# Kernel tuning notes

Hardware: AMD Instinct MI355X
Metric: run time of the kernel (lower is better)

Reference implementation:

```python
import jax, jax.numpy as jnp
import numpy as np

B, H, S, D = 2, 16, 2048, 64

def setup_inputs() -> dict:
    key = jax.random.key(0)
    kq, kk, kv = jax.random.split(key, 3)
    q = jax.random.normal(kq, (B, H, S, D), dtype=jnp.float32)
    k = jax.random.normal(kk, (B, H, S, D), dtype=jnp.float32)
    v = jax.random.normal(kv, (B, H, S, D), dtype=jnp.float32)
    # additive causal mask: 0 on/below diagonal, -1e9 above
    causal = jnp.tril(jnp.ones((S, S), dtype=bool))
    mask = jnp.where(causal, 0.0, -1e9).astype(jnp.float32)[None, None]
    return {"q": q, "k": k, "v": v, "mask": mask}

def reference(q, k, v, mask):
    # scores: [B,H,Sq,Sk]
    scale = 1.0 / jnp.sqrt(jnp.asarray(k.shape[-1], dtype=q.dtype))
    scores = jnp.einsum("bhqd,bhkd->bhqk", q, k) * scale
    scores = scores + mask
    attn = jax.nn.softmax(scores, axis=-1)
    return jnp.einsum("bhqk,bhkd->bhqd", attn, v)
```

## Files before the change

### kernel.cpp

```cpp
#include <hip/hip_runtime.h>
#include <hip/hip_bf16.h>


#define S_LEN 2048
#define D_DIM 64
#define BQ 64
#define BKV 64
#define NQT (S_LEN / BQ)
#define NBH 32

typedef __bf16 bf16x8 __attribute__((ext_vector_type(8)));
typedef __bf16 bf16x4 __attribute__((ext_vector_type(4)));
typedef float f32x4 __attribute__((ext_vector_type(4)));

#define QSCALE 0.1803368801111243f
#define NEG_INF (-1e30f)
#define THRLOG2 11.5f

__device__ inline void glds16(const void* g, void* l) {
    __builtin_amdgcn_global_load_lds(
        (const __attribute__((address_space(1))) unsigned int*)g,
        (__attribute__((address_space(3))) unsigned int*)l, 16, 0, 0);
}

__device__ inline float m3(float a, float b, float c) {
    return fmaxf(fmaxf(a, b), c);
}

__global__ __launch_bounds__(256)
void conv_fused_kernel(const float* __restrict__ k, const float* __restrict__ v,
                       __bf16* __restrict__ kb, __bf16* __restrict__ vt)
{
    __shared__ __bf16 T[64][72];
    const int bh = blockIdx.y, st = blockIdx.x;
    const int tid = threadIdx.x;
    const size_t base = (size_t)bh * S_LEN * D_DIM + (size_t)st * 64 * D_DIM;
    const float* kh = k + base;
    const float* vh = v + base;
    __bf16* kbh = kb + base;

#pragma unroll
    for (int it = 0; it < 2; ++it) {
        size_t i = ((size_t)tid + it * 256) * 8;
        float4 a = *(const float4*)(kh + i);
        float4 b = *(const float4*)(kh + i + 4);
        bf16x8 o;
        o[0] = (__bf16)a.x; o[1] = (__bf16)a.y; o[2] = (__bf16)a.z; o[3] = (__bf16)a.w;
        o[4] = (__bf16)b.x; o[5] = (__bf16)b.y; o[6] = (__bf16)b.z; o[7] = (__bf16)b.w;
        *(bf16x8*)(kbh + i) = o;
    }

#pragma unroll
    for (int it = 0; it < 4; ++it) {
        int idx = tid + it * 256;
        int s = idx >> 4, c4 = idx & 15;
        float4 f = *(const float4*)(vh + s * D_DIM + c4 * 4);
        T[c4 * 4 + 0][s] = (__bf16)f.x;
        T[c4 * 4 + 1][s] = (__bf16)f.y;
        T[c4 * 4 + 2][s] = (__bf16)f.z;
        T[c4 * 4 + 3][s] = (__bf16)f.w;
    }
    __syncthreads();
    __bf16* vth = vt + (size_t)bh * D_DIM * S_LEN + st * 64;
#pragma unroll
    for (int it = 0; it < 2; ++it) {
        int idx = tid + it * 256;
        int d = idx >> 3, c8 = idx & 7;
        int kk = c8 >> 2, g = c8 & 3;
        bf16x4 v0 = *(const bf16x4*)&T[d][kk * 32 + 4 * g];
        bf16x4 v1 = *(const bf16x4*)&T[d][kk * 32 + 16 + 4 * g];
        bf16x8 o;
        o[0] = v0[0]; o[1] = v0[1]; o[2] = v0[2]; o[3] = v0[3];
        o[4] = v1[0]; o[5] = v1[1]; o[6] = v1[2]; o[7] = v1[3];
        *(bf16x8*)(vth + (size_t)d * S_LEN + c8 * 8) = o;
    }
}


#define STAGE(kt, buf)                                                          \
    {                                                                           \
        _Pragma("unroll")                                                       \
        for (int u = 0; u < 2; ++u) {                                           \
            glds16(kh + (size_t)((kt) * BKV + row_u[u]) * D_DIM + scol_u[u],    \
                   (__bf16*)&KL[buf][0][0] + (u * 4 + w) * 512);                \
            glds16(vh + (size_t)row_u[u] * S_LEN + (kt) * BKV + scol_u[u],      \
                   (__bf16*)&VL[buf][0][0] + (u * 4 + w) * 512);                \
        }                                                                       \
    }

__global__ __launch_bounds__(256)
void attn_fwd_split(const float* __restrict__ q, const __bf16* __restrict__ kb,
                    const __bf16* __restrict__ vt, float* __restrict__ opart,
                    float* __restrict__ ml)
{
    __shared__ __bf16 KL[2][64][64];
    __shared__ __bf16 VL[2][64][64];

    const int tid  = threadIdx.x;
    const int w    = tid >> 6;
    const int lane = tid & 63;
    const int l15  = lane & 15;
    const int lg   = lane >> 4;

    const int ph = blockIdx.x;
    const int p  = ph >> 1;
    const int h  = ph & 1;
    const int bh = blockIdx.y;

    const float*  qh = q  + (size_t)bh * S_LEN * D_DIM;
    const __bf16* kh = kb + (size_t)bh * S_LEN * D_DIM;
    const __bf16* vh = vt + (size_t)bh * D_DIM * S_LEN;

    int row_u[2], scol_u[2];
#pragma unroll
    for (int u = 0; u < 2; ++u) {
        int e = (u * 4 + w) * 512 + lane * 8;
        int r = e >> 6, c0 = e & 63;
        row_u[u]  = r;
        scol_u[u] = c0 ^ ((r & 7) << 3);
    }

    for (int half = 0; half < 2; ++half) {
        const int qtile = (half == 0) ? (NQT - 1 - p) : p;
        const int qbase = qtile * BQ;
        const int cnt   = (qtile >= h) ? (((qtile - h) >> 1) + 1) : 0;

        bf16x8 qf[2];
        {
            const int qrow = qbase + w * 16 + l15;
            const float* qp = qh + (size_t)qrow * D_DIM + 8 * lg;
#pragma unroll
            for (int kk = 0; kk < 2; ++kk) {
                float4 a = *(const float4*)(qp + kk * 32);
                float4 b = *(const float4*)(qp + kk * 32 + 4);
                bf16x8 f;
                f[0] = (__bf16)(a.x * QSCALE); f[1] = (__bf16)(a.y * QSCALE);
                f[2] = (__bf16)(a.z * QSCALE); f[3] = (__bf16)(a.w * QSCALE);
                f[4] = (__bf16)(b.x * QSCALE); f[5] = (__bf16)(b.y * QSCALE);
                f[6] = (__bf16)(b.z * QSCALE); f[7] = (__bf16)(b.w * QSCALE);
                qf[kk] = f;
            }
        }

        f32x4 acc[4] = {};
        float m_run = NEG_INF;
        float l_part = 0.0f;

        if (half == 1) __syncthreads();
        if (cnt > 0) STAGE(h, 0);

        for (int i = 0; i < cnt; ++i) {
            const int kt  = h + 2 * i;
            const int cur = i & 1;
            asm volatile("s_waitcnt vmcnt(0)" ::: "memory");
            __builtin_amdgcn_s_barrier();
            if (i + 1 < cnt) STAGE(kt + 2, cur ^ 1);

            f32x4 s[4];
            __builtin_amdgcn_s_setprio(1);
#pragma unroll
            for (int jt = 0; jt < 4; ++jt) {
                const int j  = jt * 16 + l15;
                const int sw = (j & 7) << 3;
                f32x4 c = {};
#pragma unroll
                for (int kk = 0; kk < 2; ++kk) {
                    bf16x8 kf = *(const bf16x8*)&KL[cur][j][(kk * 32 + 8 * lg) ^ sw];
                    c = __builtin_amdgcn_mfma_f32_16x16x32_bf16(kf, qf[kk], c, 0, 0, 0);
                }
                s[jt] = c;
            }
            __builtin_amdgcn_s_setprio(0);

            if (kt == qtile) {
                const int qin = w * 16 + l15;
#pragma unroll
                for (int jt = 0; jt < 4; ++jt)
#pragma unroll
                    for (int r = 0; r < 4; ++r)
                        if (jt * 16 + 4 * lg + r > qin) s[jt][r] = NEG_INF;
            }

            float t0 = m3(s[0][0], s[0][1], s[0][2]);
            float t1 = m3(s[0][3], s[1][0], s[1][1]);
            float t2 = m3(s[1][2], s[1][3], s[2][0]);
            float t3 = m3(s[2][1], s[2][2], s[2][3]);
            float t4 = m3(s[3][0], s[3][1], s[3][2]);
            float mxl = m3(m3(t0, t1, t2), m3(t3, t4, s[3][3]), NEG_INF);

            if (__any(mxl > m_run + THRLOG2)) {
                float mx = fmaxf(mxl, __shfl_xor(mxl, 16));
                mx = fmaxf(mx, __shfl_xor(mx, 32));
                const float mt   = fmaxf(m_run, mx);
                const float corr = __builtin_amdgcn_exp2f(m_run - mt);
                l_part *= corr;
                m_run   = mt;
                float corr_a[4];
#pragma unroll
                for (int r = 0; r < 4; ++r) corr_a[r] = __shfl(corr, 4 * lg + r);
#pragma unroll
                for (int dt = 0; dt < 4; ++dt)
#pragma unroll
                    for (int r = 0; r < 4; ++r) acc[dt][r] *= corr_a[r];
            }

            float ps = 0.0f;
            float pe[4][4];
#pragma unroll
            for (int jt = 0; jt < 4; ++jt)
#pragma unroll
                for (int r = 0; r < 4; ++r) {
                    float e = __builtin_amdgcn_exp2f(s[jt][r] - m_run);
                    pe[jt][r] = e;
                    ps += e;
                }
            l_part += ps;

            bf16x8 pa[2];
#pragma unroll
            for (int kk = 0; kk < 2; ++kk)
#pragma unroll
                for (int i2 = 0; i2 < 4; ++i2) {
                    pa[kk][i2]     = (__bf16)pe[2 * kk][i2];
                    pa[kk][4 + i2] = (__bf16)pe[2 * kk + 1][i2];
                }

            __builtin_amdgcn_s_setprio(1);
#pragma unroll
            for (int dt = 0; dt < 4; ++dt) {
                const int d  = dt * 16 + l15;
                const int sw = (d & 7) << 3;
#pragma unroll
                for (int kk = 0; kk < 2; ++kk) {
                    bf16x8 vb = *(const bf16x8*)&VL[cur][d][(kk * 32 + 8 * lg) ^ sw];
                    acc[dt] = __builtin_amdgcn_mfma_f32_16x16x32_bf16(pa[kk], vb, acc[dt], 0, 0, 0);
                }
            }
            __builtin_amdgcn_s_setprio(0);
        }

        float l_tot = l_part + __shfl_xor(l_part, 16);
        l_tot += __shfl_xor(l_tot, 32);

        float* op = opart + ((((size_t)bh * NQT + qtile) * 2 + h) << 12);
#pragma unroll
        for (int dt = 0; dt < 4; ++dt)
#pragma unroll
            for (int r = 0; r < 4; ++r)
                op[(w * 16 + 4 * lg + r) * 64 + dt * 16 + l15] = acc[dt][r];

        if (lg == 0) {
            float* mlp = ml + ((((size_t)bh * NQT + qtile) * 2 + h) << 7);
            mlp[w * 16 + l15]      = m_run;
            mlp[64 + w * 16 + l15] = l_tot;
        }
    }
}


__global__ __launch_bounds__(256)
void combine_kernel(const float* __restrict__ opart, const float* __restrict__ ml,
                    float* __restrict__ out)
{
    const int qt  = blockIdx.x;
    const int bh  = blockIdx.y;
    const int tid = threadIdx.x;
    const int row = tid >> 2;
    const int c16 = (tid & 3) * 16;

    const float* ml0 = ml + ((((size_t)bh * NQT + qt) * 2) << 7);
    const float* ml1 = ml0 + 128;
    const float m0 = ml0[row], l0 = ml0[64 + row];
    const float m1 = ml1[row], l1 = ml1[64 + row];
    const float M  = fmaxf(m0, m1);
    const float w0 = __builtin_amdgcn_exp2f(m0 - M);
    const float w1 = __builtin_amdgcn_exp2f(m1 - M);
    const float li = __builtin_amdgcn_rcpf(w0 * l0 + w1 * l1);

    const float* o0 = opart + ((((size_t)bh * NQT + qt) * 2) << 12) + row * 64 + c16;
    const float* o1 = o0 + 4096;
    float* oh = out + ((size_t)bh * S_LEN + qt * 64 + row) * D_DIM + c16;
#pragma unroll
    for (int c = 0; c < 4; ++c) {
        float4 a = ((const float4*)o0)[c];
        float4 b = ((const float4*)o1)[c];
        float4 o;
        o.x = (a.x * w0 + b.x * w1) * li;
        o.y = (a.y * w0 + b.y * w1) * li;
        o.z = (a.z * w0 + b.z * w1) * li;
        o.w = (a.w * w0 + b.w * w1) * li;
        ((float4*)oh)[c] = o;
    }
}


__global__ __launch_bounds__(256)
void attn_fwd_glds(const float* __restrict__ q, const __bf16* __restrict__ kb,
                   const __bf16* __restrict__ vt, float* __restrict__ out)
{
    __shared__ __bf16 KL[3][64][64];
    __shared__ __bf16 VL[3][64][64];

    const int tid  = threadIdx.x;
    const int w    = tid >> 6;
    const int lane = tid & 63;
    const int l15  = lane & 15;
    const int lg   = lane >> 4;

    const int p  = blockIdx.x;
    const int bh = blockIdx.y;

    const float*  qh = q  + (size_t)bh * S_LEN * D_DIM;
    const __bf16* kh = kb + (size_t)bh * S_LEN * D_DIM;
    const __bf16* vh = vt + (size_t)bh * D_DIM * S_LEN;
    float*        oh = out + (size_t)bh * S_LEN * D_DIM;

    int row_u[2], scol_u[2];
#pragma unroll
    for (int u = 0; u < 2; ++u) {
        int e = (u * 4 + w) * 512 + lane * 8;
        int r = e >> 6, c0 = e & 63;
        row_u[u]  = r;
        scol_u[u] = c0 ^ ((r & 7) << 3);
    }

    for (int half = 0; half < 2; ++half) {
        const int qtile = (half == 0) ? (NQT - 1 - p) : p;
        const int qbase = qtile * BQ;
        const int nt    = qtile + 1;

        bf16x8 qf[2];
        {
            const int qrow = qbase + w * 16 + l15;
            const float* qp = qh + (size_t)qrow * D_DIM + 8 * lg;
#pragma unroll
            for (int kk = 0; kk < 2; ++kk) {
                float4 a = *(const float4*)(qp + kk * 32);
                float4 b = *(const float4*)(qp + kk * 32 + 4);
                bf16x8 f;
                f[0] = (__bf16)(a.x * QSCALE); f[1] = (__bf16)(a.y * QSCALE);
                f[2] = (__bf16)(a.z * QSCALE); f[3] = (__bf16)(a.w * QSCALE);
                f[4] = (__bf16)(b.x * QSCALE); f[5] = (__bf16)(b.y * QSCALE);
                f[6] = (__bf16)(b.z * QSCALE); f[7] = (__bf16)(b.w * QSCALE);
                qf[kk] = f;
            }
        }

        f32x4 acc[4] = {};
        float m_run = NEG_INF;
        float l_part = 0.0f;

        if (half == 1) __syncthreads();
        STAGE(0, 0);
        if (nt > 1) STAGE(1, 1);

        for (int kt = 0; kt < nt; ++kt) {
            const int cur = kt % 3;
            if (kt + 1 < nt) { asm volatile("s_waitcnt vmcnt(4)" ::: "memory"); }
            else             { asm volatile("s_waitcnt vmcnt(0)" ::: "memory"); }
            __builtin_amdgcn_s_barrier();
            if (kt + 2 < nt) STAGE(kt + 2, (kt + 2) % 3);

            f32x4 s[4];
            __builtin_amdgcn_s_setprio(1);
#pragma unroll
            for (int jt = 0; jt < 4; ++jt) {
                const int j  = jt * 16 + l15;
                const int sw = (j & 7) << 3;
                f32x4 c = {};
#pragma unroll
                for (int kk = 0; kk < 2; ++kk) {
                    bf16x8 kf = *(const bf16x8*)&KL[cur][j][(kk * 32 + 8 * lg) ^ sw];
                    c = __builtin_amdgcn_mfma_f32_16x16x32_bf16(kf, qf[kk], c, 0, 0, 0);
                }
                s[jt] = c;
            }
            __builtin_amdgcn_s_setprio(0);

            if (kt == qtile) {
                const int qin = w * 16 + l15;
#pragma unroll
                for (int jt = 0; jt < 4; ++jt)
#pragma unroll
                    for (int r = 0; r < 4; ++r)
                        if (jt * 16 + 4 * lg + r > qin) s[jt][r] = NEG_INF;
            }

            float t0 = m3(s[0][0], s[0][1], s[0][2]);
            float t1 = m3(s[0][3], s[1][0], s[1][1]);
            float t2 = m3(s[1][2], s[1][3], s[2][0]);
            float t3 = m3(s[2][1], s[2][2], s[2][3]);
            float t4 = m3(s[3][0], s[3][1], s[3][2]);
            float mxl = m3(m3(t0, t1, t2), m3(t3, t4, s[3][3]), NEG_INF);

            if (__any(mxl > m_run + THRLOG2)) {
                float mx = fmaxf(mxl, __shfl_xor(mxl, 16));
                mx = fmaxf(mx, __shfl_xor(mx, 32));
                const float mt   = fmaxf(m_run, mx);
                const float corr = __builtin_amdgcn_exp2f(m_run - mt);
                l_part *= corr;
                m_run   = mt;
                float corr_a[4];
#pragma unroll
                for (int r = 0; r < 4; ++r) corr_a[r] = __shfl(corr, 4 * lg + r);
#pragma unroll
                for (int dt = 0; dt < 4; ++dt)
#pragma unroll
                    for (int r = 0; r < 4; ++r) acc[dt][r] *= corr_a[r];
            }

            float ps = 0.0f;
            float pe[4][4];
#pragma unroll
            for (int jt = 0; jt < 4; ++jt)
#pragma unroll
                for (int r = 0; r < 4; ++r) {
                    float e = __builtin_amdgcn_exp2f(s[jt][r] - m_run);
                    pe[jt][r] = e;
                    ps += e;
                }
            l_part += ps;

            bf16x8 pa[2];
#pragma unroll
            for (int kk = 0; kk < 2; ++kk)
#pragma unroll
                for (int i = 0; i < 4; ++i) {
                    pa[kk][i]     = (__bf16)pe[2 * kk][i];
                    pa[kk][4 + i] = (__bf16)pe[2 * kk + 1][i];
                }

            __builtin_amdgcn_s_setprio(1);
#pragma unroll
            for (int dt = 0; dt < 4; ++dt) {
                const int d  = dt * 16 + l15;
                const int sw = (d & 7) << 3;
#pragma unroll
                for (int kk = 0; kk < 2; ++kk) {
                    bf16x8 vb = *(const bf16x8*)&VL[cur][d][(kk * 32 + 8 * lg) ^ sw];
                    acc[dt] = __builtin_amdgcn_mfma_f32_16x16x32_bf16(pa[kk], vb, acc[dt], 0, 0, 0);
                }
            }
            __builtin_amdgcn_s_setprio(0);
        }

        float l_tot = l_part + __shfl_xor(l_part, 16);
        l_tot += __shfl_xor(l_tot, 32);
        float li_a[4];
#pragma unroll
        for (int r = 0; r < 4; ++r)
            li_a[r] = __builtin_amdgcn_rcpf(__shfl(l_tot, 4 * lg + r));
#pragma unroll
        for (int dt = 0; dt < 4; ++dt)
#pragma unroll
            for (int r = 0; r < 4; ++r)
                oh[(size_t)(qbase + w * 16 + 4 * lg + r) * D_DIM + dt * 16 + l15] =
                    acc[dt][r] * li_a[r];
    }
}
#undef STAGE


#define PAD 72
__global__ __launch_bounds__(256)
void attn_fwd_fallback(const float* __restrict__ q, const float* __restrict__ k,
                       const float* __restrict__ v, float* __restrict__ out)
{
    __shared__ __bf16 Klds[64][PAD];
    __shared__ __bf16 Vt[D_DIM][PAD];
    __shared__ __bf16 Plds[4][16][PAD];

    const int tid  = threadIdx.x;
    const int w    = tid >> 6;
    const int lane = tid & 63;
    const int l15  = lane & 15;
    const int lg   = lane >> 4;

    const int qtile = blockIdx.x;
    const int bh    = blockIdx.y;
    const int qbase = qtile * 64;

    const size_t head_off = (size_t)bh * S_LEN * D_DIM;
    const float* qh = q + head_off;
    const float* kh = k + head_off;
    const float* vh = v + head_off;
    float*       oh = out + head_off;

    bf16x8 qf[2];
    {
        const int qrow = qbase + w * 16 + l15;
        const float* qp = qh + (size_t)qrow * D_DIM + 8 * lg;
#pragma unroll
        for (int c = 0; c < 2; ++c) {
            float4 a = *(const float4*)(qp + c * 32);
            float4 b = *(const float4*)(qp + c * 32 + 4);
            bf16x8 f;
            f[0] = (__bf16)(a.x * 0.125f); f[1] = (__bf16)(a.y * 0.125f);
            f[2] = (__bf16)(a.z * 0.125f); f[3] = (__bf16)(a.w * 0.125f);
            f[4] = (__bf16)(b.x * 0.125f); f[5] = (__bf16)(b.y * 0.125f);
            f[6] = (__bf16)(b.z * 0.125f); f[7] = (__bf16)(b.w * 0.125f);
            qf[c] = f;
        }
    }

    f32x4 acc[4] = {};
    float m_run[4], l_run[4];
#pragma unroll
    for (int r = 0; r < 4; ++r) { m_run[r] = -1e30f; l_run[r] = 0.0f; }

    const int nkv = qtile + 1;
    for (int kt = 0; kt < nkv; ++kt) {
        const int kv0 = kt * 64;
        __syncthreads();
#pragma unroll
        for (int it = 0; it < 4; ++it) {
            int idx = tid + it * 256;
            int row = idx >> 4;
            int c4  = idx & 15;
            float4 kf = *(const float4*)(kh + (size_t)(kv0 + row) * D_DIM + c4 * 4);
            __bf16* kd = &Klds[row][c4 * 4];
            kd[0] = (__bf16)kf.x; kd[1] = (__bf16)kf.y;
            kd[2] = (__bf16)kf.z; kd[3] = (__bf16)kf.w;
            float4 vf = *(const float4*)(vh + (size_t)(kv0 + row) * D_DIM + c4 * 4);
            Vt[c4 * 4 + 0][row] = (__bf16)vf.x;
            Vt[c4 * 4 + 1][row] = (__bf16)vf.y;
            Vt[c4 * 4 + 2][row] = (__bf16)vf.z;
            Vt[c4 * 4 + 3][row] = (__bf16)vf.w;
        }
        __syncthreads();

        f32x4 sfrag[4];
#pragma unroll
        for (int kc = 0; kc < 4; ++kc) {
            bf16x8 kf0 = *(const bf16x8*)&Klds[kc * 16 + l15][8 * lg];
            bf16x8 kf1 = *(const bf16x8*)&Klds[kc * 16 + l15][32 + 8 * lg];
            f32x4 c = {};
            c = __builtin_amdgcn_mfma_f32_16x16x32_bf16(qf[0], kf0, c, 0, 0, 0);
            c = __builtin_amdgcn_mfma_f32_16x16x32_bf16(qf[1], kf1, c, 0, 0, 0);
            sfrag[kc] = c;
        }

        if (kt == qtile) {
#pragma unroll
            for (int kc = 0; kc < 4; ++kc) {
                const int j = kv0 + kc * 16 + l15;
#pragma unroll
                for (int r = 0; r < 4; ++r) {
                    const int qrow = qbase + w * 16 + lg * 4 + r;
                    if (j > qrow) sfrag[kc][r] = -1e30f;
                }
            }
        }

        float mt[4], corr[4], ps[4];
#pragma unroll
        for (int r = 0; r < 4; ++r) {
            float mx = fmaxf(fmaxf(sfrag[0][r], sfrag[1][r]),
                             fmaxf(sfrag[2][r], sfrag[3][r]));
            mx = fmaxf(mx, __shfl_xor(mx, 1));
            mx = fmaxf(mx, __shfl_xor(mx, 2));
            mx = fmaxf(mx, __shfl_xor(mx, 4));
            mx = fmaxf(mx, __shfl_xor(mx, 8));
            mt[r]   = fmaxf(m_run[r], mx);
            corr[r] = __expf(m_run[r] - mt[r]);
            ps[r]   = 0.0f;
        }
#pragma unroll
        for (int kc = 0; kc < 4; ++kc) {
#pragma unroll
            for (int r = 0; r < 4; ++r) {
                float pp = __expf(sfrag[kc][r] - mt[r]);
                ps[r] += pp;
                Plds[w][lg * 4 + r][kc * 16 + l15] = (__bf16)pp;
            }
        }
#pragma unroll
        for (int r = 0; r < 4; ++r) {
            ps[r] += __shfl_xor(ps[r], 1);
            ps[r] += __shfl_xor(ps[r], 2);
            ps[r] += __shfl_xor(ps[r], 4);
            ps[r] += __shfl_xor(ps[r], 8);
            l_run[r] = l_run[r] * corr[r] + ps[r];
            m_run[r] = mt[r];
        }
#pragma unroll
        for (int dt = 0; dt < 4; ++dt)
#pragma unroll
            for (int r = 0; r < 4; ++r)
                acc[dt][r] *= corr[r];

#pragma unroll
        for (int kk = 0; kk < 2; ++kk) {
            bf16x8 pf = *(const bf16x8*)&Plds[w][l15][kk * 32 + 8 * lg];
#pragma unroll
            for (int dt = 0; dt < 4; ++dt) {
                bf16x8 vf = *(const bf16x8*)&Vt[dt * 16 + l15][kk * 32 + 8 * lg];
                acc[dt] = __builtin_amdgcn_mfma_f32_16x16x32_bf16(pf, vf, acc[dt], 0, 0, 0);
            }
        }
    }

#pragma unroll
    for (int dt = 0; dt < 4; ++dt) {
#pragma unroll
        for (int r = 0; r < 4; ++r) {
            const int qrow = qbase + w * 16 + lg * 4 + r;
            oh[(size_t)qrow * D_DIM + dt * 16 + l15] = acc[dt][r] / l_run[r];
        }
    }
}

extern "C" void kernel_launch(void* const* d_in, const int* in_sizes, int n_in,
                              void* d_out, int out_size, void* d_ws, size_t ws_size,
                              hipStream_t stream) {
    const float* q = (const float*)d_in[0];
    const float* k = (const float*)d_in[1];
    const float* v = (const float*)d_in[2];
    float* out = (float*)d_out;

    const size_t kv_elems   = (size_t)NBH * S_LEN * D_DIM;
    const size_t conv_bytes = kv_elems * 2 * sizeof(__bf16);
    const size_t op_bytes   = (size_t)NBH * NQT * 2 * 4096 * 4;
    const size_t ml_bytes   = (size_t)NBH * NQT * 2 * 128 * 4;

    if (ws_size >= conv_bytes + op_bytes + ml_bytes) {
        __bf16* kb = (__bf16*)d_ws;
        __bf16* vt = kb + kv_elems;
        float* opart = (float*)((char*)d_ws + conv_bytes);
        float* ml    = (float*)((char*)d_ws + conv_bytes + op_bytes);
        conv_fused_kernel<<<dim3(S_LEN / 64, NBH), dim3(256), 0, stream>>>(k, v, kb, vt);
        attn_fwd_split<<<dim3(32, NBH), dim3(256), 0, stream>>>(q, kb, vt, opart, ml);
        combine_kernel<<<dim3(NQT, NBH), dim3(256), 0, stream>>>(opart, ml, out);
    } else if (ws_size >= conv_bytes) {
        __bf16* kb = (__bf16*)d_ws;
        __bf16* vt = kb + kv_elems;
        conv_fused_kernel<<<dim3(S_LEN / 64, NBH), dim3(256), 0, stream>>>(k, v, kb, vt);
        attn_fwd_glds<<<dim3(NQT / 2, NBH), dim3(256), 0, stream>>>(q, kb, vt, out);
    } else {
        attn_fwd_fallback<<<dim3(S_LEN / 64, NBH), dim3(256), 0, stream>>>(q, k, v, out);
    }
}
```

Baseline: 60.33 us.

## Split attention into one q-tile per block, triple-buffer KV, store partials as bf16

Each block of the split kernel now handles a single query tile and KV parity instead of a paired long and short tile, doubling the grid to 64x32 blocks. The K/V LDS staging moves from double to triple buffering with a partial vmcnt wait, so two tiles are in flight. Partial outputs are stored as bf16 rather than fp32, which halves the partial write and combine read traffic. The cost is less even per-block work across the causal triangle, more LDS per block, and some extra rounding of the partial outputs.

```diff
diff --git a/kernel.cpp b/kernel.cpp
--- a/kernel.cpp
+++ b/kernel.cpp
@@ -90,11 +90,11 @@
 
 __global__ __launch_bounds__(256)
 void attn_fwd_split(const float* __restrict__ q, const __bf16* __restrict__ kb,
-                    const __bf16* __restrict__ vt, float* __restrict__ opart,
+                    const __bf16* __restrict__ vt, __bf16* __restrict__ opart,
                     float* __restrict__ ml)
 {
-    __shared__ __bf16 KL[2][64][64];
-    __shared__ __bf16 VL[2][64][64];
+    __shared__ __bf16 KL[3][64][64];
+    __shared__ __bf16 VL[3][64][64];
 
     const int tid  = threadIdx.x;
     const int w    = tid >> 6;
@@ -102,10 +102,12 @@
     const int l15  = lane & 15;
     const int lg   = lane >> 4;
 
-    const int ph = blockIdx.x;
-    const int p  = ph >> 1;
-    const int h  = ph & 1;
-    const int bh = blockIdx.y;
+    const int u0    = blockIdx.x;
+    const int qtile = NQT - 1 - (u0 >> 1);
+    const int h     = u0 & 1;
+    const int bh    = blockIdx.y;
+    const int qbase = qtile * BQ;
+    const int cnt   = (qtile >= h) ? (((qtile - h) >> 1) + 1) : 0;
 
     const float*  qh = q  + (size_t)bh * S_LEN * D_DIM;
     const __bf16* kh = kb + (size_t)bh * S_LEN * D_DIM;
@@ -120,146 +122,141 @@
         scol_u[u] = c0 ^ ((r & 7) << 3);
     }
 
-    for (int half = 0; half < 2; ++half) {
-        const int qtile = (half == 0) ? (NQT - 1 - p) : p;
-        const int qbase = qtile * BQ;
-        const int cnt   = (qtile >= h) ? (((qtile - h) >> 1) + 1) : 0;
-
-        bf16x8 qf[2];
-        {
-            const int qrow = qbase + w * 16 + l15;
-            const float* qp = qh + (size_t)qrow * D_DIM + 8 * lg;
+    bf16x8 qf[2];
+    {
+        const int qrow = qbase + w * 16 + l15;
+        const float* qp = qh + (size_t)qrow * D_DIM + 8 * lg;
+#pragma unroll
+        for (int kk = 0; kk < 2; ++kk) {
+            float4 a = *(const float4*)(qp + kk * 32);
+            float4 b = *(const float4*)(qp + kk * 32 + 4);
+            bf16x8 f;
+            f[0] = (__bf16)(a.x * QSCALE); f[1] = (__bf16)(a.y * QSCALE);
+            f[2] = (__bf16)(a.z * QSCALE); f[3] = (__bf16)(a.w * QSCALE);
+            f[4] = (__bf16)(b.x * QSCALE); f[5] = (__bf16)(b.y * QSCALE);
+            f[6] = (__bf16)(b.z * QSCALE); f[7] = (__bf16)(b.w * QSCALE);
+            qf[kk] = f;
+        }
+    }
+
+    f32x4 acc[4] = {};
+    float m_run = NEG_INF;
+    float l_part = 0.0f;
+
+    if (cnt > 0) STAGE(h, 0);
+    if (cnt > 1) STAGE(h + 2, 1);
+
+    for (int i = 0; i < cnt; ++i) {
+        const int kt  = h + 2 * i;
+        const int cur = i % 3;
+        if (i + 1 < cnt) { asm volatile("s_waitcnt vmcnt(4)" ::: "memory"); }
+        else             { asm volatile("s_waitcnt vmcnt(0)" ::: "memory"); }
+        __builtin_amdgcn_s_barrier();
+        if (i + 2 < cnt) STAGE(h + 2 * (i + 2), (i + 2) % 3);
+
+        f32x4 s[4];
+        __builtin_amdgcn_s_setprio(1);
+#pragma unroll
+        for (int jt = 0; jt < 4; ++jt) {
+            const int j  = jt * 16 + l15;
+            const int sw = (j & 7) << 3;
+            f32x4 c = {};
 #pragma unroll
             for (int kk = 0; kk < 2; ++kk) {
-                float4 a = *(const float4*)(qp + kk * 32);
-                float4 b = *(const float4*)(qp + kk * 32 + 4);
-                bf16x8 f;
-                f[0] = (__bf16)(a.x * QSCALE); f[1] = (__bf16)(a.y * QSCALE);
-                f[2] = (__bf16)(a.z * QSCALE); f[3] = (__bf16)(a.w * QSCALE);
-                f[4] = (__bf16)(b.x * QSCALE); f[5] = (__bf16)(b.y * QSCALE);
-                f[6] = (__bf16)(b.z * QSCALE); f[7] = (__bf16)(b.w * QSCALE);
-                qf[kk] = f;
-            }
-        }
-
-        f32x4 acc[4] = {};
-        float m_run = NEG_INF;
-        float l_part = 0.0f;
-
-        if (half == 1) __syncthreads();
-        if (cnt > 0) STAGE(h, 0);
-
-        for (int i = 0; i < cnt; ++i) {
-            const int kt  = h + 2 * i;
-            const int cur = i & 1;
-            asm volatile("s_waitcnt vmcnt(0)" ::: "memory");
-            __builtin_amdgcn_s_barrier();
-            if (i + 1 < cnt) STAGE(kt + 2, cur ^ 1);
-
-            f32x4 s[4];
-            __builtin_amdgcn_s_setprio(1);
-#pragma unroll
-            for (int jt = 0; jt < 4; ++jt) {
-                const int j  = jt * 16 + l15;
-                const int sw = (j & 7) << 3;
-                f32x4 c = {};
-#pragma unroll
-                for (int kk = 0; kk < 2; ++kk) {
-                    bf16x8 kf = *(const bf16x8*)&KL[cur][j][(kk * 32 + 8 * lg) ^ sw];
-                    c = __builtin_amdgcn_mfma_f32_16x16x32_bf16(kf, qf[kk], c, 0, 0, 0);
-                }
-                s[jt] = c;
-            }
-            __builtin_amdgcn_s_setprio(0);
-
-            if (kt == qtile) {
-                const int qin = w * 16 + l15;
-#pragma unroll
-                for (int jt = 0; jt < 4; ++jt)
-#pragma unroll
-                    for (int r = 0; r < 4; ++r)
-                        if (jt * 16 + 4 * lg + r > qin) s[jt][r] = NEG_INF;
-            }
-
-            float t0 = m3(s[0][0], s[0][1], s[0][2]);
-            float t1 = m3(s[0][3], s[1][0], s[1][1]);
-            float t2 = m3(s[1][2], s[1][3], s[2][0]);
-            float t3 = m3(s[2][1], s[2][2], s[2][3]);
-            float t4 = m3(s[3][0], s[3][1], s[3][2]);
-            float mxl = m3(m3(t0, t1, t2), m3(t3, t4, s[3][3]), NEG_INF);
-
-            if (__any(mxl > m_run + THRLOG2)) {
-                float mx = fmaxf(mxl, __shfl_xor(mxl, 16));
-                mx = fmaxf(mx, __shfl_xor(mx, 32));
-                const float mt   = fmaxf(m_run, mx);
-                const float corr = __builtin_amdgcn_exp2f(m_run - mt);
-                l_part *= corr;
-                m_run   = mt;
-                float corr_a[4];
-#pragma unroll
-                for (int r = 0; r < 4; ++r) corr_a[r] = __shfl(corr, 4 * lg + r);
-#pragma unroll
-                for (int dt = 0; dt < 4; ++dt)
-#pragma unroll
-                    for (int r = 0; r < 4; ++r) acc[dt][r] *= corr_a[r];
-            }
-
-            float ps = 0.0f;
-            float pe[4][4];
+                bf16x8 kf = *(const bf16x8*)&KL[cur][j][(kk * 32 + 8 * lg) ^ sw];
+                c = __builtin_amdgcn_mfma_f32_16x16x32_bf16(kf, qf[kk], c, 0, 0, 0);
+            }
+            s[jt] = c;
+        }
+        __builtin_amdgcn_s_setprio(0);
+
+        if (kt == qtile) {
+            const int qin = w * 16 + l15;
 #pragma unroll
             for (int jt = 0; jt < 4; ++jt)
 #pragma unroll
-                for (int r = 0; r < 4; ++r) {
-                    float e = __builtin_amdgcn_exp2f(s[jt][r] - m_run);
-                    pe[jt][r] = e;
-                    ps += e;
-                }
-            l_part += ps;
-
-            bf16x8 pa[2];
-#pragma unroll
-            for (int kk = 0; kk < 2; ++kk)
-#pragma unroll
-                for (int i2 = 0; i2 < 4; ++i2) {
-                    pa[kk][i2]     = (__bf16)pe[2 * kk][i2];
-                    pa[kk][4 + i2] = (__bf16)pe[2 * kk + 1][i2];
-                }
-
-            __builtin_amdgcn_s_setprio(1);
-#pragma unroll
-            for (int dt = 0; dt < 4; ++dt) {
-                const int d  = dt * 16 + l15;
-                const int sw = (d & 7) << 3;
-#pragma unroll
-                for (int kk = 0; kk < 2; ++kk) {
-                    bf16x8 vb = *(const bf16x8*)&VL[cur][d][(kk * 32 + 8 * lg) ^ sw];
-                    acc[dt] = __builtin_amdgcn_mfma_f32_16x16x32_bf16(pa[kk], vb, acc[dt], 0, 0, 0);
-                }
-            }
-            __builtin_amdgcn_s_setprio(0);
-        }
-
-        float l_tot = l_part + __shfl_xor(l_part, 16);
-        l_tot += __shfl_xor(l_tot, 32);
-
-        float* op = opart + ((((size_t)bh * NQT + qtile) * 2 + h) << 12);
-#pragma unroll
-        for (int dt = 0; dt < 4; ++dt)
-#pragma unroll
-            for (int r = 0; r < 4; ++r)
-                op[(w * 16 + 4 * lg + r) * 64 + dt * 16 + l15] = acc[dt][r];
-
-        if (lg == 0) {
-            float* mlp = ml + ((((size_t)bh * NQT + qtile) * 2 + h) << 7);
-            mlp[w * 16 + l15]      = m_run;
-            mlp[64 + w * 16 + l15] = l_tot;
-        }
+                for (int r = 0; r < 4; ++r)
+                    if (jt * 16 + 4 * lg + r > qin) s[jt][r] = NEG_INF;
+        }
+
+        float t0 = m3(s[0][0], s[0][1], s[0][2]);
+        float t1 = m3(s[0][3], s[1][0], s[1][1]);
+        float t2 = m3(s[1][2], s[1][3], s[2][0]);
+        float t3 = m3(s[2][1], s[2][2], s[2][3]);
+        float t4 = m3(s[3][0], s[3][1], s[3][2]);
+        float mxl = m3(m3(t0, t1, t2), m3(t3, t4, s[3][3]), NEG_INF);
+
+        if (__any(mxl > m_run + THRLOG2)) {
+            float mx = fmaxf(mxl, __shfl_xor(mxl, 16));
+            mx = fmaxf(mx, __shfl_xor(mx, 32));
+            const float mt   = fmaxf(m_run, mx);
+            const float corr = __builtin_amdgcn_exp2f(m_run - mt);
+            l_part *= corr;
+            m_run   = mt;
+            float corr_a[4];
+#pragma unroll
+            for (int r = 0; r < 4; ++r) corr_a[r] = __shfl(corr, 4 * lg + r);
+#pragma unroll
+            for (int dt = 0; dt < 4; ++dt)
+#pragma unroll
+                for (int r = 0; r < 4; ++r) acc[dt][r] *= corr_a[r];
+        }
+
+        float ps = 0.0f;
+        float pe[4][4];
+#pragma unroll
+        for (int jt = 0; jt < 4; ++jt)
+#pragma unroll
+            for (int r = 0; r < 4; ++r) {
+                float e = __builtin_amdgcn_exp2f(s[jt][r] - m_run);
+                pe[jt][r] = e;
+                ps += e;
+            }
+        l_part += ps;
+
+        bf16x8 pa[2];
+#pragma unroll
+        for (int kk = 0; kk < 2; ++kk)
+#pragma unroll
+            for (int i2 = 0; i2 < 4; ++i2) {
+                pa[kk][i2]     = (__bf16)pe[2 * kk][i2];
+                pa[kk][4 + i2] = (__bf16)pe[2 * kk + 1][i2];
+            }
+
+        __builtin_amdgcn_s_setprio(1);
+#pragma unroll
+        for (int dt = 0; dt < 4; ++dt) {
+            const int d  = dt * 16 + l15;
+            const int sw = (d & 7) << 3;
+#pragma unroll
+            for (int kk = 0; kk < 2; ++kk) {
+                bf16x8 vb = *(const bf16x8*)&VL[cur][d][(kk * 32 + 8 * lg) ^ sw];
+                acc[dt] = __builtin_amdgcn_mfma_f32_16x16x32_bf16(pa[kk], vb, acc[dt], 0, 0, 0);
+            }
+        }
+        __builtin_amdgcn_s_setprio(0);
+    }
+
+    float l_tot = l_part + __shfl_xor(l_part, 16);
+    l_tot += __shfl_xor(l_tot, 32);
+
+    __bf16* op = opart + ((((size_t)bh * NQT + qtile) * 2 + h) << 12);
+#pragma unroll
+    for (int dt = 0; dt < 4; ++dt)
+#pragma unroll
+        for (int r = 0; r < 4; ++r)
+            op[(w * 16 + 4 * lg + r) * 64 + dt * 16 + l15] = (__bf16)acc[dt][r];
+
+    if (lg == 0) {
+        float* mlp = ml + ((((size_t)bh * NQT + qtile) * 2 + h) << 7);
+        mlp[w * 16 + l15]      = m_run;
+        mlp[64 + w * 16 + l15] = l_tot;
     }
 }
 
 
 __global__ __launch_bounds__(256)
-void combine_kernel(const float* __restrict__ opart, const float* __restrict__ ml,
+void combine_kernel(const __bf16* __restrict__ opart, const float* __restrict__ ml,
                     float* __restrict__ out)
 {
     const int qt  = blockIdx.x;
@@ -277,20 +274,23 @@
     const float w1 = __builtin_amdgcn_exp2f(m1 - M);
     const float li = __builtin_amdgcn_rcpf(w0 * l0 + w1 * l1);
 
-    const float* o0 = opart + ((((size_t)bh * NQT + qt) * 2) << 12) + row * 64 + c16;
-    const float* o1 = o0 + 4096;
+    const __bf16* o0 = opart + ((((size_t)bh * NQT + qt) * 2) << 12) + row * 64 + c16;
+    const __bf16* o1 = o0 + 4096;
+    bf16x8 a0 = *(const bf16x8*)o0;
+    bf16x8 a1 = *(const bf16x8*)(o0 + 8);
+    bf16x8 b0 = *(const bf16x8*)o1;
+    bf16x8 b1 = *(const bf16x8*)(o1 + 8);
+
     float* oh = out + ((size_t)bh * S_LEN + qt * 64 + row) * D_DIM + c16;
-#pragma unroll
-    for (int c = 0; c < 4; ++c) {
-        float4 a = ((const float4*)o0)[c];
-        float4 b = ((const float4*)o1)[c];
-        float4 o;
-        o.x = (a.x * w0 + b.x * w1) * li;
-        o.y = (a.y * w0 + b.y * w1) * li;
-        o.z = (a.z * w0 + b.z * w1) * li;
-        o.w = (a.w * w0 + b.w * w1) * li;
-        ((float4*)oh)[c] = o;
-    }
+    float res[16];
+#pragma unroll
+    for (int j = 0; j < 8; ++j) {
+        res[j]     = ((float)a0[j] * w0 + (float)b0[j] * w1) * li;
+        res[8 + j] = ((float)a1[j] * w0 + (float)b1[j] * w1) * li;
+    }
+#pragma unroll
+    for (int c = 0; c < 4; ++c)
+        ((float4*)oh)[c] = make_float4(res[c*4], res[c*4+1], res[c*4+2], res[c*4+3]);
 }
 
 
@@ -620,16 +620,16 @@
 
     const size_t kv_elems   = (size_t)NBH * S_LEN * D_DIM;
     const size_t conv_bytes = kv_elems * 2 * sizeof(__bf16);
-    const size_t op_bytes   = (size_t)NBH * NQT * 2 * 4096 * 4;
+    const size_t op_bytes   = (size_t)NBH * NQT * 2 * 4096 * 2;
     const size_t ml_bytes   = (size_t)NBH * NQT * 2 * 128 * 4;
 
     if (ws_size >= conv_bytes + op_bytes + ml_bytes) {
         __bf16* kb = (__bf16*)d_ws;
         __bf16* vt = kb + kv_elems;
-        float* opart = (float*)((char*)d_ws + conv_bytes);
-        float* ml    = (float*)((char*)d_ws + conv_bytes + op_bytes);
+        __bf16* opart = (__bf16*)((char*)d_ws + conv_bytes);
+        float*  ml    = (float*)((char*)d_ws + conv_bytes + op_bytes);
         conv_fused_kernel<<<dim3(S_LEN / 64, NBH), dim3(256), 0, stream>>>(k, v, kb, vt);
-        attn_fwd_split<<<dim3(32, NBH), dim3(256), 0, stream>>>(q, kb, vt, opart, ml);
+        attn_fwd_split<<<dim3(64, NBH), dim3(256), 0, stream>>>(q, kb, vt, opart, ml);
         combine_kernel<<<dim3(NQT, NBH), dim3(256), 0, stream>>>(opart, ml, out);
     } else if (ws_size >= conv_bytes) {
         __bf16* kb = (__bf16*)d_ws;
```

Measured after the change: 70.62 us. 1.17x slower.

## Use 128-row Q tiles per block in split attention with bf16 partial outputs

Applied to the files above, without the earlier changes.

The split attention kernel now processes 128 query rows per block, with each wave handling two 16-row chunks. Each K/V tile loaded into LDS is therefore reused across twice as many queries, and the paired-tile load balancing is replaced by launching the longest tiles first. Partial outputs are stored as bf16 instead of fp32 to halve the workspace traffic into the combine kernel, and launch bounds now request 4 blocks per SM. The trade-offs are higher register pressure and some extra rounding error in the partial outputs.

```diff
diff --git a/kernel.cpp b/kernel.cpp
--- a/kernel.cpp
+++ b/kernel.cpp
@@ -4,17 +4,17 @@
 
 #define S_LEN 2048
 #define D_DIM 64
-#define BQ 64
 #define BKV 64
-#define NQT (S_LEN / BQ)
 #define NBH 32
+#define NT128 16
 
 typedef __bf16 bf16x8 __attribute__((ext_vector_type(8)));
 typedef __bf16 bf16x4 __attribute__((ext_vector_type(4)));
 typedef float f32x4 __attribute__((ext_vector_type(4)));
 
 #define QSCALE 0.1803368801111243f
-#define NEG_INF (-1e30f)
+#define NEG_MASK (-1e30f)
+#define M_INIT  (-1e29f)
 #define THRLOG2 11.5f
 
 __device__ inline void glds16(const void* g, void* l) {
@@ -88,9 +88,10 @@
         }                                                                       \
     }
 
-__global__ __launch_bounds__(256)
+
+__global__ __launch_bounds__(256, 4)
 void attn_fwd_split(const float* __restrict__ q, const __bf16* __restrict__ kb,
-                    const __bf16* __restrict__ vt, float* __restrict__ opart,
+                    const __bf16* __restrict__ vt, __bf16* __restrict__ opart,
                     float* __restrict__ ml)
 {
     __shared__ __bf16 KL[2][64][64];
@@ -102,10 +103,12 @@
     const int l15  = lane & 15;
     const int lg   = lane >> 4;
 
-    const int ph = blockIdx.x;
-    const int p  = ph >> 1;
-    const int h  = ph & 1;
+    const int u0 = blockIdx.x;
+    const int T  = NT128 - 1 - (u0 >> 1);
+    const int h  = u0 & 1;
     const int bh = blockIdx.y;
+    const int qbase = T * 128;
+    const int cnt   = T + 1;
 
     const float*  qh = q  + (size_t)bh * S_LEN * D_DIM;
     const __bf16* kh = kb + (size_t)bh * S_LEN * D_DIM;
@@ -120,10 +123,244 @@
         scol_u[u] = c0 ^ ((r & 7) << 3);
     }
 
+    bf16x8 qf[2][2];
+#pragma unroll
+    for (int qc = 0; qc < 2; ++qc) {
+        const int qrow = qbase + w * 32 + qc * 16 + l15;
+        const float* qp = qh + (size_t)qrow * D_DIM + 8 * lg;
+#pragma unroll
+        for (int kk = 0; kk < 2; ++kk) {
+            float4 a = *(const float4*)(qp + kk * 32);
+            float4 b = *(const float4*)(qp + kk * 32 + 4);
+            bf16x8 f;
+            f[0] = (__bf16)(a.x * QSCALE); f[1] = (__bf16)(a.y * QSCALE);
+            f[2] = (__bf16)(a.z * QSCALE); f[3] = (__bf16)(a.w * QSCALE);
+            f[4] = (__bf16)(b.x * QSCALE); f[5] = (__bf16)(b.y * QSCALE);
+            f[6] = (__bf16)(b.z * QSCALE); f[7] = (__bf16)(b.w * QSCALE);
+            qf[qc][kk] = f;
+        }
+    }
+
+    f32x4 acc[4][2] = {};
+    float m_run[2]  = {M_INIT, M_INIT};
+    float l_part[2] = {0.0f, 0.0f};
+
+    STAGE(h, 0);
+
+    for (int i = 0; i < cnt; ++i) {
+        const int kt  = h + 2 * i;
+        const int cur = i & 1;
+        asm volatile("s_waitcnt vmcnt(0)" ::: "memory");
+        __builtin_amdgcn_s_barrier();
+        if (i + 1 < cnt) STAGE(kt + 2, cur ^ 1);
+
+        bf16x8 kf[4][2];
+#pragma unroll
+        for (int jt = 0; jt < 4; ++jt) {
+            const int j  = jt * 16 + l15;
+            const int sw = (j & 7) << 3;
+            kf[jt][0] = *(const bf16x8*)&KL[cur][j][(8 * lg) ^ sw];
+            kf[jt][1] = *(const bf16x8*)&KL[cur][j][(32 + 8 * lg) ^ sw];
+        }
+
+        f32x4 s0[4], s1[4];
+        __builtin_amdgcn_s_setprio(1);
+#pragma unroll
+        for (int jt = 0; jt < 4; ++jt) {
+            f32x4 c = {};
+            c = __builtin_amdgcn_mfma_f32_16x16x32_bf16(kf[jt][0], qf[0][0], c, 0, 0, 0);
+            c = __builtin_amdgcn_mfma_f32_16x16x32_bf16(kf[jt][1], qf[0][1], c, 0, 0, 0);
+            s0[jt] = c;
+            f32x4 d = {};
+            d = __builtin_amdgcn_mfma_f32_16x16x32_bf16(kf[jt][0], qf[1][0], d, 0, 0, 0);
+            d = __builtin_amdgcn_mfma_f32_16x16x32_bf16(kf[jt][1], qf[1][1], d, 0, 0, 0);
+            s1[jt] = d;
+        }
+        __builtin_amdgcn_s_setprio(0);
+
+        if (i == cnt - 1) {
+            const int q0 = w * 32 + l15;
+#pragma unroll
+            for (int jt = 0; jt < 4; ++jt)
+#pragma unroll
+                for (int r = 0; r < 4; ++r) {
+                    const int jl = h * 64 + jt * 16 + 4 * lg + r;
+                    if (jl > q0)      s0[jt][r] = NEG_MASK;
+                    if (jl > q0 + 16) s1[jt][r] = NEG_MASK;
+                }
+        }
+
+        float mxl0, mxl1;
+        {
+            float t0 = m3(s0[0][0], s0[0][1], s0[0][2]);
+            float t1 = m3(s0[0][3], s0[1][0], s0[1][1]);
+            float t2 = m3(s0[1][2], s0[1][3], s0[2][0]);
+            float t3 = m3(s0[2][1], s0[2][2], s0[2][3]);
+            float t4 = m3(s0[3][0], s0[3][1], s0[3][2]);
+            mxl0 = m3(m3(t0, t1, t2), m3(t3, t4, s0[3][3]), NEG_MASK);
+            float u1 = m3(s1[0][0], s1[0][1], s1[0][2]);
+            float u2 = m3(s1[0][3], s1[1][0], s1[1][1]);
+            float u3 = m3(s1[1][2], s1[1][3], s1[2][0]);
+            float u4 = m3(s1[2][1], s1[2][2], s1[2][3]);
+            float u5 = m3(s1[3][0], s1[3][1], s1[3][2]);
+            mxl1 = m3(m3(u1, u2, u3), m3(u4, u5, s1[3][3]), NEG_MASK);
+        }
+
+        if (__any((mxl0 > m_run[0] + THRLOG2) || (mxl1 > m_run[1] + THRLOG2))) {
+            float mx0 = fmaxf(mxl0, __shfl_xor(mxl0, 16));
+            mx0 = fmaxf(mx0, __shfl_xor(mx0, 32));
+            float mx1 = fmaxf(mxl1, __shfl_xor(mxl1, 16));
+            mx1 = fmaxf(mx1, __shfl_xor(mx1, 32));
+            const float mt0 = fmaxf(m_run[0], mx0);
+            const float mt1 = fmaxf(m_run[1], mx1);
+            const float c0 = __builtin_amdgcn_exp2f(m_run[0] - mt0);
+            const float c1 = __builtin_amdgcn_exp2f(m_run[1] - mt1);
+            l_part[0] *= c0; m_run[0] = mt0;
+            l_part[1] *= c1; m_run[1] = mt1;
+            float ca0[4], ca1[4];
+#pragma unroll
+            for (int r = 0; r < 4; ++r) {
+                ca0[r] = __shfl(c0, 4 * lg + r);
+                ca1[r] = __shfl(c1, 4 * lg + r);
+            }
+#pragma unroll
+            for (int dt = 0; dt < 4; ++dt)
+#pragma unroll
+                for (int r = 0; r < 4; ++r) {
+                    acc[dt][0][r] *= ca0[r];
+                    acc[dt][1][r] *= ca1[r];
+                }
+        }
+
+        float ps0 = 0.0f, ps1 = 0.0f;
+        bf16x8 pa0[2], pa1[2];
+#pragma unroll
+        for (int kk = 0; kk < 2; ++kk)
+#pragma unroll
+            for (int i2 = 0; i2 < 4; ++i2) {
+                float ea = __builtin_amdgcn_exp2f(s0[2 * kk][i2] - m_run[0]);
+                float eb = __builtin_amdgcn_exp2f(s0[2 * kk + 1][i2] - m_run[0]);
+                ps0 += ea + eb;
+                pa0[kk][i2]     = (__bf16)ea;
+                pa0[kk][4 + i2] = (__bf16)eb;
+                float fa = __builtin_amdgcn_exp2f(s1[2 * kk][i2] - m_run[1]);
+                float fb = __builtin_amdgcn_exp2f(s1[2 * kk + 1][i2] - m_run[1]);
+                ps1 += fa + fb;
+                pa1[kk][i2]     = (__bf16)fa;
+                pa1[kk][4 + i2] = (__bf16)fb;
+            }
+        l_part[0] += ps0;
+        l_part[1] += ps1;
+
+        __builtin_amdgcn_s_setprio(1);
+#pragma unroll
+        for (int dt = 0; dt < 4; ++dt) {
+            const int d  = dt * 16 + l15;
+            const int sw = (d & 7) << 3;
+#pragma unroll
+            for (int kk = 0; kk < 2; ++kk) {
+                bf16x8 vb = *(const bf16x8*)&VL[cur][d][(kk * 32 + 8 * lg) ^ sw];
+                acc[dt][0] = __builtin_amdgcn_mfma_f32_16x16x32_bf16(pa0[kk], vb, acc[dt][0], 0, 0, 0);
+                acc[dt][1] = __builtin_amdgcn_mfma_f32_16x16x32_bf16(pa1[kk], vb, acc[dt][1], 0, 0, 0);
+            }
+        }
+        __builtin_amdgcn_s_setprio(0);
+    }
+
+    __bf16* op  = opart + ((((size_t)bh * NT128 + T) * 2 + h) << 13);
+    float*  mlp = ml    + ((((size_t)bh * NT128 + T) * 2 + h) << 8);
+#pragma unroll
+    for (int qc = 0; qc < 2; ++qc) {
+        float lt = l_part[qc] + __shfl_xor(l_part[qc], 16);
+        lt += __shfl_xor(lt, 32);
+#pragma unroll
+        for (int dt = 0; dt < 4; ++dt)
+#pragma unroll
+            for (int r = 0; r < 4; ++r)
+                op[(w * 32 + qc * 16 + 4 * lg + r) * 64 + dt * 16 + l15] =
+                    (__bf16)acc[dt][qc][r];
+        if (lg == 0) {
+            mlp[w * 32 + qc * 16 + l15]       = m_run[qc];
+            mlp[128 + w * 32 + qc * 16 + l15] = lt;
+        }
+    }
+}
+
+
+__global__ __launch_bounds__(256)
+void combine_kernel(const __bf16* __restrict__ opart, const float* __restrict__ ml,
+                    float* __restrict__ out)
+{
+    const int T   = blockIdx.x;
+    const int bh  = blockIdx.y;
+    const int tid = threadIdx.x;
+    const int row = tid >> 1;
+    const int c0  = (tid & 1) * 32;
+
+    const float* mlp = ml + (((size_t)bh * NT128 + T) * 2 << 8);
+    const float m0 = mlp[row],       l0 = mlp[128 + row];
+    const float m1 = mlp[256 + row], l1 = mlp[384 + row];
+    const float M  = fmaxf(m0, m1);
+    const float w0 = __builtin_amdgcn_exp2f(m0 - M);
+    const float w1 = __builtin_amdgcn_exp2f(m1 - M);
+    const float li = __builtin_amdgcn_rcpf(w0 * l0 + w1 * l1);
+
+    const __bf16* o0 = opart + (((size_t)bh * NT128 + T) * 2 << 13) + row * 64 + c0;
+    const __bf16* o1 = o0 + 8192;
+    float* oh = out + ((size_t)bh * S_LEN + T * 128 + row) * D_DIM + c0;
+#pragma unroll
+    for (int cc = 0; cc < 4; ++cc) {
+        bf16x8 a = *(const bf16x8*)(o0 + cc * 8);
+        bf16x8 b = *(const bf16x8*)(o1 + cc * 8);
+        float4 r0, r1;
+        r0.x = ((float)a[0] * w0 + (float)b[0] * w1) * li;
+        r0.y = ((float)a[1] * w0 + (float)b[1] * w1) * li;
+        r0.z = ((float)a[2] * w0 + (float)b[2] * w1) * li;
+        r0.w = ((float)a[3] * w0 + (float)b[3] * w1) * li;
+        r1.x = ((float)a[4] * w0 + (float)b[4] * w1) * li;
+        r1.y = ((float)a[5] * w0 + (float)b[5] * w1) * li;
+        r1.z = ((float)a[6] * w0 + (float)b[6] * w1) * li;
+        r1.w = ((float)a[7] * w0 + (float)b[7] * w1) * li;
+        ((float4*)(oh + cc * 8))[0] = r0;
+        ((float4*)(oh + cc * 8))[1] = r1;
+    }
+}
+
+
+__global__ __launch_bounds__(256)
+void attn_fwd_glds(const float* __restrict__ q, const __bf16* __restrict__ kb,
+                   const __bf16* __restrict__ vt, float* __restrict__ out)
+{
+    __shared__ __bf16 KL[3][64][64];
+    __shared__ __bf16 VL[3][64][64];
+
+    const int tid  = threadIdx.x;
+    const int w    = tid >> 6;
+    const int lane = tid & 63;
+    const int l15  = lane & 15;
+    const int lg   = lane >> 4;
+
+    const int p  = blockIdx.x;
+    const int bh = blockIdx.y;
+
+    const float*  qh = q  + (size_t)bh * S_LEN * D_DIM;
+    const __bf16* kh = kb + (size_t)bh * S_LEN * D_DIM;
+    const __bf16* vh = vt + (size_t)bh * D_DIM * S_LEN;
+    float*        oh = out + (size_t)bh * S_LEN * D_DIM;
+
+    int row_u[2], scol_u[2];
+#pragma unroll
+    for (int u = 0; u < 2; ++u) {
+        int e = (u * 4 + w) * 512 + lane * 8;
+        int r = e >> 6, c0 = e & 63;
+        row_u[u]  = r;
+        scol_u[u] = c0 ^ ((r & 7) << 3);
+    }
+
     for (int half = 0; half < 2; ++half) {
-        const int qtile = (half == 0) ? (NQT - 1 - p) : p;
-        const int qbase = qtile * BQ;
-        const int cnt   = (qtile >= h) ? (((qtile - h) >> 1) + 1) : 0;
+        const int qtile = (half == 0) ? (31 - p) : p;
+        const int qbase = qtile * 64;
+        const int nt    = qtile + 1;
 
         bf16x8 qf[2];
         {
@@ -143,211 +380,7 @@
         }
 
         f32x4 acc[4] = {};
-        float m_run = NEG_INF;
-        float l_part = 0.0f;
-
-        if (half == 1) __syncthreads();
-        if (cnt > 0) STAGE(h, 0);
-
-        for (int i = 0; i < cnt; ++i) {
-            const int kt  = h + 2 * i;
-            const int cur = i & 1;
-            asm volatile("s_waitcnt vmcnt(0)" ::: "memory");
-            __builtin_amdgcn_s_barrier();
-            if (i + 1 < cnt) STAGE(kt + 2, cur ^ 1);
-
-            f32x4 s[4];
-            __builtin_amdgcn_s_setprio(1);
-#pragma unroll
-            for (int jt = 0; jt < 4; ++jt) {
-                const int j  = jt * 16 + l15;
-                const int sw = (j & 7) << 3;
-                f32x4 c = {};
-#pragma unroll
-                for (int kk = 0; kk < 2; ++kk) {
-                    bf16x8 kf = *(const bf16x8*)&KL[cur][j][(kk * 32 + 8 * lg) ^ sw];
-                    c = __builtin_amdgcn_mfma_f32_16x16x32_bf16(kf, qf[kk], c, 0, 0, 0);
-                }
-                s[jt] = c;
-            }
-            __builtin_amdgcn_s_setprio(0);
-
-            if (kt == qtile) {
-                const int qin = w * 16 + l15;
-#pragma unroll
-                for (int jt = 0; jt < 4; ++jt)
-#pragma unroll
-                    for (int r = 0; r < 4; ++r)
-                        if (jt * 16 + 4 * lg + r > qin) s[jt][r] = NEG_INF;
-            }
-
-            float t0 = m3(s[0][0], s[0][1], s[0][2]);
-            float t1 = m3(s[0][3], s[1][0], s[1][1]);
-            float t2 = m3(s[1][2], s[1][3], s[2][0]);
-            float t3 = m3(s[2][1], s[2][2], s[2][3]);
-            float t4 = m3(s[3][0], s[3][1], s[3][2]);
-            float mxl = m3(m3(t0, t1, t2), m3(t3, t4, s[3][3]), NEG_INF);
-
-            if (__any(mxl > m_run + THRLOG2)) {
-                float mx = fmaxf(mxl, __shfl_xor(mxl, 16));
-                mx = fmaxf(mx, __shfl_xor(mx, 32));
-                const float mt   = fmaxf(m_run, mx);
-                const float corr = __builtin_amdgcn_exp2f(m_run - mt);
-                l_part *= corr;
-                m_run   = mt;
-                float corr_a[4];
-#pragma unroll
-                for (int r = 0; r < 4; ++r) corr_a[r] = __shfl(corr, 4 * lg + r);
-#pragma unroll
-                for (int dt = 0; dt < 4; ++dt)
-#pragma unroll
-                    for (int r = 0; r < 4; ++r) acc[dt][r] *= corr_a[r];
-            }
-
-            float ps = 0.0f;
-            float pe[4][4];
-#pragma unroll
-            for (int jt = 0; jt < 4; ++jt)
-#pragma unroll
-                for (int r = 0; r < 4; ++r) {
-                    float e = __builtin_amdgcn_exp2f(s[jt][r] - m_run);
-                    pe[jt][r] = e;
-                    ps += e;
-                }
-            l_part += ps;
-
-            bf16x8 pa[2];
-#pragma unroll
-            for (int kk = 0; kk < 2; ++kk)
-#pragma unroll
-                for (int i2 = 0; i2 < 4; ++i2) {
-                    pa[kk][i2]     = (__bf16)pe[2 * kk][i2];
-                    pa[kk][4 + i2] = (__bf16)pe[2 * kk + 1][i2];
-                }
-
-            __builtin_amdgcn_s_setprio(1);
-#pragma unroll
-            for (int dt = 0; dt < 4; ++dt) {
-                const int d  = dt * 16 + l15;
-                const int sw = (d & 7) << 3;
-#pragma unroll
-                for (int kk = 0; kk < 2; ++kk) {
-                    bf16x8 vb = *(const bf16x8*)&VL[cur][d][(kk * 32 + 8 * lg) ^ sw];
-                    acc[dt] = __builtin_amdgcn_mfma_f32_16x16x32_bf16(pa[kk], vb, acc[dt], 0, 0, 0);
-                }
-            }
-            __builtin_amdgcn_s_setprio(0);
-        }
-
-        float l_tot = l_part + __shfl_xor(l_part, 16);
-        l_tot += __shfl_xor(l_tot, 32);
-
-        float* op = opart + ((((size_t)bh * NQT + qtile) * 2 + h) << 12);
-#pragma unroll
-        for (int dt = 0; dt < 4; ++dt)
-#pragma unroll
-            for (int r = 0; r < 4; ++r)
-                op[(w * 16 + 4 * lg + r) * 64 + dt * 16 + l15] = acc[dt][r];
-
-        if (lg == 0) {
-            float* mlp = ml + ((((size_t)bh * NQT + qtile) * 2 + h) << 7);
-            mlp[w * 16 + l15]      = m_run;
-            mlp[64 + w * 16 + l15] = l_tot;
-        }
-    }
-}
-
-
-__global__ __launch_bounds__(256)
-void combine_kernel(const float* __restrict__ opart, const float* __restrict__ ml,
-                    float* __restrict__ out)
-{
-    const int qt  = blockIdx.x;
-    const int bh  = blockIdx.y;
-    const int tid = threadIdx.x;
-    const int row = tid >> 2;
-    const int c16 = (tid & 3) * 16;
-
-    const float* ml0 = ml + ((((size_t)bh * NQT + qt) * 2) << 7);
-    const float* ml1 = ml0 + 128;
-    const float m0 = ml0[row], l0 = ml0[64 + row];
-    const float m1 = ml1[row], l1 = ml1[64 + row];
-    const float M  = fmaxf(m0, m1);
-    const float w0 = __builtin_amdgcn_exp2f(m0 - M);
-    const float w1 = __builtin_amdgcn_exp2f(m1 - M);
-    const float li = __builtin_amdgcn_rcpf(w0 * l0 + w1 * l1);
-
-    const float* o0 = opart + ((((size_t)bh * NQT + qt) * 2) << 12) + row * 64 + c16;
-    const float* o1 = o0 + 4096;
-    float* oh = out + ((size_t)bh * S_LEN + qt * 64 + row) * D_DIM + c16;
-#pragma unroll
-    for (int c = 0; c < 4; ++c) {
-        float4 a = ((const float4*)o0)[c];
-        float4 b = ((const float4*)o1)[c];
-        float4 o;
-        o.x = (a.x * w0 + b.x * w1) * li;
-        o.y = (a.y * w0 + b.y * w1) * li;
-        o.z = (a.z * w0 + b.z * w1) * li;
-        o.w = (a.w * w0 + b.w * w1) * li;
-        ((float4*)oh)[c] = o;
-    }
-}
-
-
-__global__ __launch_bounds__(256)
-void attn_fwd_glds(const float* __restrict__ q, const __bf16* __restrict__ kb,
-                   const __bf16* __restrict__ vt, float* __restrict__ out)
-{
-    __shared__ __bf16 KL[3][64][64];
-    __shared__ __bf16 VL[3][64][64];
-
-    const int tid  = threadIdx.x;
-    const int w    = tid >> 6;
-    const int lane = tid & 63;
-    const int l15  = lane & 15;
-    const int lg   = lane >> 4;
-
-    const int p  = blockIdx.x;
-    const int bh = blockIdx.y;
-
-    const float*  qh = q  + (size_t)bh * S_LEN * D_DIM;
-    const __bf16* kh = kb + (size_t)bh * S_LEN * D_DIM;
-    const __bf16* vh = vt + (size_t)bh * D_DIM * S_LEN;
-    float*        oh = out + (size_t)bh * S_LEN * D_DIM;
-
-    int row_u[2], scol_u[2];
-#pragma unroll
-    for (int u = 0; u < 2; ++u) {
-        int e = (u * 4 + w) * 512 + lane * 8;
-        int r = e >> 6, c0 = e & 63;
-        row_u[u]  = r;
-        scol_u[u] = c0 ^ ((r & 7) << 3);
-    }
-
-    for (int half = 0; half < 2; ++half) {
-        const int qtile = (half == 0) ? (NQT - 1 - p) : p;
-        const int qbase = qtile * BQ;
-        const int nt    = qtile + 1;
-
-        bf16x8 qf[2];
-        {
-            const int qrow = qbase + w * 16 + l15;
-            const float* qp = qh + (size_t)qrow * D_DIM + 8 * lg;
-#pragma unroll
-            for (int kk = 0; kk < 2; ++kk) {
-                float4 a = *(const float4*)(qp + kk * 32);
-                float4 b = *(const float4*)(qp + kk * 32 + 4);
-                bf16x8 f;
-                f[0] = (__bf16)(a.x * QSCALE); f[1] = (__bf16)(a.y * QSCALE);
-                f[2] = (__bf16)(a.z * QSCALE); f[3] = (__bf16)(a.w * QSCALE);
-                f[4] = (__bf16)(b.x * QSCALE); f[5] = (__bf16)(b.y * QSCALE);
-                f[6] = (__bf16)(b.z * QSCALE); f[7] = (__bf16)(b.w * QSCALE);
-                qf[kk] = f;
-            }
-        }
-
-        f32x4 acc[4] = {};
-        float m_run = NEG_INF;
+        float m_run = M_INIT;
         float l_part = 0.0f;
 
         if (half == 1) __syncthreads();
@@ -383,7 +416,7 @@
                 for (int jt = 0; jt < 4; ++jt)
 #pragma unroll
                     for (int r = 0; r < 4; ++r)
-                        if (jt * 16 + 4 * lg + r > qin) s[jt][r] = NEG_INF;
+                        if (jt * 16 + 4 * lg + r > qin) s[jt][r] = NEG_MASK;
             }
 
             float t0 = m3(s[0][0], s[0][1], s[0][2]);
@@ -391,7 +424,7 @@
             float t2 = m3(s[1][2], s[1][3], s[2][0]);
             float t3 = m3(s[2][1], s[2][2], s[2][3]);
             float t4 = m3(s[3][0], s[3][1], s[3][2]);
-            float mxl = m3(m3(t0, t1, t2), m3(t3, t4, s[3][3]), NEG_INF);
+            float mxl = m3(m3(t0, t1, t2), m3(t3, t4, s[3][3]), NEG_MASK);
 
             if (__any(mxl > m_run + THRLOG2)) {
                 float mx = fmaxf(mxl, __shfl_xor(mxl, 16));
@@ -620,22 +653,22 @@
 
     const size_t kv_elems   = (size_t)NBH * S_LEN * D_DIM;
     const size_t conv_bytes = kv_elems * 2 * sizeof(__bf16);
-    const size_t op_bytes   = (size_t)NBH * NQT * 2 * 4096 * 4;
-    const size_t ml_bytes   = (size_t)NBH * NQT * 2 * 128 * 4;
+    const size_t op_bytes   = (size_t)NBH * NT128 * 2 * 8192 * 2;
+    const size_t ml_bytes   = (size_t)NBH * NT128 * 2 * 256 * 4;
 
     if (ws_size >= conv_bytes + op_bytes + ml_bytes) {
         __bf16* kb = (__bf16*)d_ws;
         __bf16* vt = kb + kv_elems;
-        float* opart = (float*)((char*)d_ws + conv_bytes);
-        float* ml    = (float*)((char*)d_ws + conv_bytes + op_bytes);
+        __bf16* opart = (__bf16*)((char*)d_ws + conv_bytes);
+        float*  ml    = (float*)((char*)d_ws + conv_bytes + op_bytes);
         conv_fused_kernel<<<dim3(S_LEN / 64, NBH), dim3(256), 0, stream>>>(k, v, kb, vt);
         attn_fwd_split<<<dim3(32, NBH), dim3(256), 0, stream>>>(q, kb, vt, opart, ml);
-        combine_kernel<<<dim3(NQT, NBH), dim3(256), 0, stream>>>(opart, ml, out);
+        combine_kernel<<<dim3(NT128, NBH), dim3(256), 0, stream>>>(opart, ml, out);
     } else if (ws_size >= conv_bytes) {
         __bf16* kb = (__bf16*)d_ws;
         __bf16* vt = kb + kv_elems;
         conv_fused_kernel<<<dim3(S_LEN / 64, NBH), dim3(256), 0, stream>>>(k, v, kb, vt);
-        attn_fwd_glds<<<dim3(NQT / 2, NBH), dim3(256), 0, stream>>>(q, kb, vt, out);
+        attn_fwd_glds<<<dim3(16, NBH), dim3(256), 0, stream>>>(q, kb, vt, out);
     } else {
         attn_fwd_fallback<<<dim3(S_LEN / 64, NBH), dim3(256), 0, stream>>>(q, k, v, out);
     }
```

New measurement: 65.00 us. 1.08x slower.
